# Kernel optimization log

Hardware: AMD Instinct MI355X
Metric: run time of the kernel (lower is better)

Reference implementation:

```python
import jax, jax.numpy as jnp
import numpy as np

EPS_BN = 1e-5
EPS_RENORM = 1e-9

def conv_bn_relu(x, W, g, b, m, v):
    # x: [B, Cin, N], W: [Cout, Cin] (1x1 conv, no bias). Eval-mode BN.
    y = jnp.einsum('oi,bin->bon', W, x)
    scale = (g / jnp.sqrt(v + EPS_BN))[None, :, None]
    bias = (b - m * g / jnp.sqrt(v + EPS_BN))[None, :, None]
    return jax.nn.relu(y * scale + bias)

def _make_params(key, cout, cin):
    k1, k2, k3, k4 = jax.random.split(key, 4)
    W = jax.random.normal(k1, (cout, cin), jnp.float32) * (1.0 / np.sqrt(cin))
    g = jax.random.uniform(k2, (cout,), jnp.float32, 0.5, 1.5)
    b = jax.random.normal(k3, (cout,), jnp.float32) * 0.1
    m = jax.random.normal(k4, (cout,), jnp.float32) * 0.1
    v = jax.random.uniform(jax.random.fold_in(key, 7), (cout,), jnp.float32, 0.5, 1.5)
    return W, g, b, m, v

def setup_inputs() -> dict:
    key = jax.random.key(0)
    ks = jax.random.split(key, 6)
    B, C, N = 8, 1024, 2048
    x = jax.random.normal(ks[0], (B, C, N), jnp.float32)
    inp = {'x': x}
    dims = [(1024, 1024), (1024, 1024), (128, 1024), (128, 1024), (1024, 1024)]
    for i, (co, ci) in enumerate(dims):
        W, g, b, m, v = _make_params(ks[i + 1], co, ci)
        inp[f'W{i+1}'] = W
        inp[f'g{i+1}'] = g
        inp[f'b{i+1}'] = b
        inp[f'm{i+1}'] = m
        inp[f'v{i+1}'] = v
    return inp

def reference(x,
              W1, g1, b1, m1, v1,
              W2, g2, b2, m2, v2,
              W3, g3, b3, m3, v3,
              W4, g4, b4, m4, v4,
              W5, g5, b5, m5, v5):
    x1 = conv_bn_relu(x, W1, g1, b1, m1, v1)          # [B,1024,N]
    v_ = conv_bn_relu(x1, W2, g2, b2, m2, v2)         # [B,1024,N]
    q_ = conv_bn_relu(x1, W3, g3, b3, m3, v3)         # [B,128,N]
    k_ = conv_bn_relu(x1, W4, g4, b4, m4, v4)         # [B,128,N]
    # q transposed: [B,N,128] @ [B,128,N] -> [B,N,N]
    scores = jnp.einsum('bcn,bcm->bnm', q_, k_)
    scores = jax.nn.softmax(scores, axis=-1)
    scores = scores / (EPS_RENORM + scores.sum(axis=1, keepdims=True))
    attn = jnp.einsum('bcn,bnm->bcm', v_, scores)     # [B,1024,N]
    x2 = conv_bn_relu(x1 - attn, W5, g5, b5, m5, v5)
    return x1 + x2
```

## Files before the change

kernel.cpp:

```cpp
#include <hip/hip_runtime.h>

typedef unsigned short u16;
using bf16x8 = __attribute__((ext_vector_type(8))) short;
using f32x4  = __attribute__((ext_vector_type(4))) float;

#define CH   1024
#define NP   2048
#define CQ   128

__device__ __forceinline__ float bf2f(u16 u){
  union { unsigned u; float f; } c; c.u = ((unsigned)u) << 16; return c.f;
}
__device__ __forceinline__ u16 f2bf(float f){
  unsigned x = __float_as_uint(f);
  unsigned r = (x + 0x7fffu + ((x >> 16) & 1u)) >> 16;
  return (u16)r;
}

__device__ __forceinline__ void gl2lds16(const u16* g, u16* l){
  __builtin_amdgcn_global_load_lds(
      (const __attribute__((address_space(1))) unsigned int*)(const void*)g,
      (__attribute__((address_space(3))) unsigned int*)(void*)l,
      16, 0, 0);
}

__global__ void ws_marker(float* out, float have_mb){
  out[0] = 1048576.0f + have_mb;
}

__global__ __launch_bounds__(256) void transpose_split(const float* __restrict__ x,
                                                       u16* __restrict__ xh,
                                                       u16* __restrict__ xl){
  const int bb = blockIdx.z;
  const int n0 = blockIdx.x * 64, c0 = blockIdx.y * 64;
  __shared__ float tile[64][65];
  const int t = threadIdx.x;
  const float* xb = x + ((size_t)bb*CH + c0)*NP + n0;
#pragma unroll
  for (int rr = 0; rr < 4; ++rr){
    const int c_l = (t >> 4) + rr*16;
    const int n_l = (t & 15) * 4;
    float4 v = *(const float4*)&xb[(size_t)c_l*NP + n_l];
    tile[c_l][n_l+0] = v.x; tile[c_l][n_l+1] = v.y;
    tile[c_l][n_l+2] = v.z; tile[c_l][n_l+3] = v.w;
  }
  __syncthreads();
  u16* oh = xh + ((size_t)bb*NP + n0)*CH + c0;
  u16* ol = xl + ((size_t)bb*NP + n0)*CH + c0;
#pragma unroll
  for (int rr = 0; rr < 4; ++rr){
    const int n_l = (t >> 4) + rr*16;
    const int c_l = (t & 15) * 4;
    ushort4 h, l;
    float v0 = tile[c_l+0][n_l], v1 = tile[c_l+1][n_l];
    float v2 = tile[c_l+2][n_l], v3 = tile[c_l+3][n_l];
    h.x = f2bf(v0); l.x = f2bf(v0 - bf2f(h.x));
    h.y = f2bf(v1); l.y = f2bf(v1 - bf2f(h.y));
    h.z = f2bf(v2); l.z = f2bf(v2 - bf2f(h.z));
    h.w = f2bf(v3); l.w = f2bf(v3 - bf2f(h.w));
    *(ushort4*)&oh[(size_t)n_l*CH + c_l] = h;
    *(ushort4*)&ol[(size_t)n_l*CH + c_l] = l;
  }
}

__global__ __launch_bounds__(256) void prep_all(
    const float* __restrict__ w0, const float* __restrict__ w1,
    const float* __restrict__ w2, const float* __restrict__ w3,
    const float* __restrict__ w4,
    u16* w1h, u16* w1l, u16* w2h,
    u16* w34h, u16* w34l, u16* w5h,
    const float* g3, const float* b3, const float* m3, const float* v3,
    const float* g4, const float* b4, const float* m4, const float* v4,
    float* p34, float* colsum){
  const int seg = blockIdx.y;
  if (seg == 5){
    for (int i = blockIdx.x*blockDim.x + threadIdx.x; i < 1024; i += gridDim.x*blockDim.x){
      const int grp = i >> 8, j = i & 255;
      const float* pa = (grp==0) ? g3 : (grp==1) ? b3 : (grp==2) ? m3 : v3;
      const float* pb = (grp==0) ? g4 : (grp==1) ? b4 : (grp==2) ? m4 : v4;
      p34[i] = (j < 128) ? pa[j] : pb[j-128];
    }
    return;
  }
  if (seg == 6){
    for (int i = blockIdx.x*blockDim.x + threadIdx.x; i < 8*NP; i += gridDim.x*blockDim.x)
      colsum[i] = 0.f;
    return;
  }
  const float* w; u16 *wh, *wl; int n;
  switch (seg){
    case 0:  w = w0; wh = w1h;           wl = w1l;           n = CH*CH; break;
    case 1:  w = w1; wh = w2h;           wl = nullptr;       n = CH*CH; break;
    case 2:  w = w2; wh = w34h;          wl = w34l;          n = CQ*CH; break;
    case 3:  w = w3; wh = w34h + CQ*CH;  wl = w34l + CQ*CH;  n = CQ*CH; break;
    default: w = w4; wh = w5h;           wl = nullptr;       n = CH*CH; break;
  }
  for (int i = blockIdx.x*blockDim.x + threadIdx.x; i < n; i += gridDim.x*blockDim.x){
    float v = w[i];
    u16 h = f2bf(v);
    wh[i] = h;
    if (wl) wl[i] = f2bf(v - bf2f(h));
  }
}

template<int EPI>
__global__ __launch_bounds__(512, 2) void gemm_2ph(
    const u16* __restrict__ A, const u16* __restrict__ B,
    int lda, int ldb, long astr, long bstr, int K,
    void* __restrict__ out0, long ostr, int ldo,
    const float* __restrict__ pg, const float* __restrict__ pb,
    const float* __restrict__ pm, const float* __restrict__ pv,
    const u16* __restrict__ x1h, const u16* __restrict__ x1l,
    const float* __restrict__ cinv, const u16* __restrict__ cbf)
{
  __shared__ __align__(16) u16 sA[2][16384];
  __shared__ __align__(16) u16 sB[2][16384];
  __shared__ __align__(16) u16 cl[2048];

  const int tid  = threadIdx.x;
  const int lane = tid & 63;
  const int wave = tid >> 6;
  const int wr = wave >> 1, wc = wave & 1;
  const int l15 = lane & 15, q = lane >> 4;
  const int id = blockIdx.x;
  const int bb = id & 7;
  const int rest = id >> 3;
  const int by = rest & 3;
  const int bx = rest >> 2;

  const u16* Ab = A + (size_t)bb*astr + (size_t)bx*256*lda;
  const u16* Bb = B + (size_t)bb*bstr + (size_t)by*256*ldb;

  const int sr0 = tid >> 3;
  const int sg  = (((tid & 7) ^ (sr0 & 7)) << 3);

  auto stage = [&](int kt, int bsel){
    u16* dA = sA[bsel]; u16* dB = sB[bsel];
#pragma unroll
    for (int rr = 0; rr < 4; ++rr){
      gl2lds16(Ab + (size_t)(rr*64 + sr0)*lda + kt + sg, dA + rr*4096 + tid*8);
      gl2lds16(Bb + (size_t)(rr*64 + sr0)*ldb + kt + sg, dB + rr*4096 + tid*8);
    }
  };

  int rpA[4], rpB[8];
#pragma unroll
  for (int i = 0; i < 4; ++i) rpA[i] = (wr*64 + i*16 + l15) << 6;
#pragma unroll
  for (int j = 0; j < 8; ++j) rpB[j] = (wc*128 + j*16 + l15) << 6;
  const int ckx = l15 & 7;
  const int ck0 = ((0 + q) ^ ckx) << 3;
  const int ck1 = ((4 + q) ^ ckx) << 3;

  if constexpr (EPI == 1){
    if (tid < 256)
      *(bf16x8*)&cl[tid*8] = *(const bf16x8*)&cbf[(size_t)bb*NP + tid*8];
  }

  f32x4 acc[4][8] = {};
  f32x4 accR[4] = {};

  const int NT = K >> 6;
  stage(0, 0);
  __syncthreads();

  for (int t = 0; t < NT; ++t){
    if (t + 1 < NT) stage((t + 1) << 6, (t + 1) & 1);
    const u16* cA = sA[t & 1];
    const u16* cB = sB[t & 1];
    bf16x8 af[4], bfr[8];
#pragma unroll
    for (int i = 0; i < 4; ++i) af[i]  = *(const bf16x8*)&cA[rpA[i] + ck0];
#pragma unroll
    for (int j = 0; j < 8; ++j) bfr[j] = *(const bf16x8*)&cB[rpB[j] + ck0];
    if constexpr (EPI == 1){
      const bf16x8 cbs = *(const bf16x8*)&cl[(t << 6) + q*8];
#pragma unroll
      for (int i = 0; i < 4; ++i)
        accR[i] = __builtin_amdgcn_mfma_f32_16x16x32_bf16(af[i], cbs, accR[i], 0, 0, 0);
    }
#pragma unroll
    for (int i = 0; i < 4; ++i)
#pragma unroll
      for (int j = 0; j < 8; ++j)
        acc[i][j] = __builtin_amdgcn_mfma_f32_16x16x32_bf16(af[i], bfr[j], acc[i][j], 0, 0, 0);
#pragma unroll
    for (int i = 0; i < 4; ++i) af[i]  = *(const bf16x8*)&cA[rpA[i] + ck1];
#pragma unroll
    for (int j = 0; j < 8; ++j) bfr[j] = *(const bf16x8*)&cB[rpB[j] + ck1];
    if constexpr (EPI == 1){
      const bf16x8 cbs = *(const bf16x8*)&cl[(t << 6) + 32 + q*8];
#pragma unroll
      for (int i = 0; i < 4; ++i)
        accR[i] = __builtin_amdgcn_mfma_f32_16x16x32_bf16(af[i], cbs, accR[i], 0, 0, 0);
    }
#pragma unroll
    for (int i = 0; i < 4; ++i)
#pragma unroll
      for (int j = 0; j < 8; ++j)
        acc[i][j] = __builtin_amdgcn_mfma_f32_16x16x32_bf16(af[i], bfr[j], acc[i][j], 0, 0, 0);
    __syncthreads();
  }

  const int rbase = bx*256 + wr*64;
  const int cbase = by*256 + wc*128;
#pragma unroll
  for (int j = 0; j < 8; ++j){
    const int gc = cbase + j*16 + l15;
    float scale = 0.f, bias = 0.f;
    if (EPI == 0 || EPI == 2){
      scale = pg[gc] * rsqrtf(pv[gc] + 1e-5f);
      bias  = pb[gc] - pm[gc]*scale;
    }
#pragma unroll
    for (int i = 0; i < 4; ++i){
      const int gr0 = rbase + i*16 + q*4;
      if (EPI == 0){
        const float4 cv = *(const float4*)&cinv[(size_t)bb*NP + gr0];
        ushort4 pk;
        pk.x = f2bf(fmaxf(acc[i][j][0]*scale + bias, 0.f) * cv.x);
        pk.y = f2bf(fmaxf(acc[i][j][1]*scale + bias, 0.f) * cv.y);
        pk.z = f2bf(fmaxf(acc[i][j][2]*scale + bias, 0.f) * cv.z);
        pk.w = f2bf(fmaxf(acc[i][j][3]*scale + bias, 0.f) * cv.w);
        *(ushort4*)&((u16*)out0)[(size_t)bb*ostr + (size_t)gc*ldo + gr0] = pk;
      } else if (EPI == 1){
#pragma unroll
        for (int r = 0; r < 4; ++r){
          const int gr = gr0 + r;
          const size_t idx = (size_t)bb*ostr + (size_t)gr*ldo + gc;
          const float rsv = 1.f / (1e-9f + accR[i][r]);
          const float x1v = bf2f(x1h[idx]) + bf2f(x1l[idx]);
          ((u16*)out0)[idx] = f2bf(x1v - acc[i][j][r]*rsv);
        }
      } else {
        float4 o4;
#pragma unroll
        for (int r = 0; r < 4; ++r){
          const int gr = gr0 + r;
          const size_t xidx = (size_t)bb*((size_t)NP*CH) + (size_t)gr*CH + gc;
          const float x2  = fmaxf(acc[i][j][r]*scale + bias, 0.f);
          const float x1v = bf2f(x1h[xidx]) + bf2f(x1l[xidx]);
          (&o4.x)[r] = x1v + x2;
        }
        *(float4*)&((float*)out0)[(size_t)bb*ostr + (size_t)gc*ldo + gr0] = o4;
      }
    }
  }
}

__global__ __launch_bounds__(512, 2) void gemm_split_big(
    const u16* __restrict__ Ah, const u16* __restrict__ Al,
    const u16* __restrict__ Bh, const u16* __restrict__ Bl,
    int lda, int ldb, long astr, long bstr, int K,
    u16* __restrict__ outH, u16* __restrict__ outL,
    long ostr, int ldo,
    const float* __restrict__ pg, const float* __restrict__ pb,
    const float* __restrict__ pm, const float* __restrict__ pv)
{
  __shared__ __align__(16) u16 sAh[2][8192], sAl[2][8192];
  __shared__ __align__(16) u16 sBh[2][8192], sBl[2][8192];

  const int tid  = threadIdx.x;
  const int lane = tid & 63;
  const int wave = tid >> 6;
  const int wr = wave >> 1, wc = wave & 1;
  const int l15 = lane & 15, q = lane >> 4;
  const int id = blockIdx.x;
  const int bb = id & 7;
  const int rest = id >> 3;
  const int by = rest & 3;
  const int bx = rest >> 2;

  const u16* Abh = Ah + (size_t)bb*astr + (size_t)bx*256*lda;
  const u16* Abl = Al + (size_t)bb*astr + (size_t)bx*256*lda;
  const u16* Bbh = Bh + (size_t)bb*bstr + (size_t)by*256*ldb;
  const u16* Bbl = Bl + (size_t)bb*bstr + (size_t)by*256*ldb;

  const int sr = tid >> 2;
  const int sg = (((tid & 3) ^ ((sr >> 1) & 3)) << 3);

  auto stage = [&](int kt, int bsel){
    gl2lds16(Abh + (size_t)sr*lda        + kt + sg, &sAh[bsel][tid*8]);
    gl2lds16(Abh + (size_t)(sr+128)*lda  + kt + sg, &sAh[bsel][4096 + tid*8]);
    gl2lds16(Abl + (size_t)sr*lda        + kt + sg, &sAl[bsel][tid*8]);
    gl2lds16(Abl + (size_t)(sr+128)*lda  + kt + sg, &sAl[bsel][4096 + tid*8]);
    gl2lds16(Bbh + (size_t)sr*ldb        + kt + sg, &sBh[bsel][tid*8]);
    gl2lds16(Bbh + (size_t)(sr+128)*ldb  + kt + sg, &sBh[bsel][4096 + tid*8]);
    gl2lds16(Bbl + (size_t)sr*ldb        + kt + sg, &sBl[bsel][tid*8]);
    gl2lds16(Bbl + (size_t)(sr+128)*ldb  + kt + sg, &sBl[bsel][4096 + tid*8]);
  };

  int offA[4], offB[8];
#pragma unroll
  for (int i = 0; i < 4; ++i){
    const int ra = wr*64 + i*16 + l15;
    offA[i] = ra*32 + ((q ^ ((ra >> 1) & 3)) << 3);
  }
#pragma unroll
  for (int j = 0; j < 8; ++j){
    const int rb = wc*128 + j*16 + l15;
    offB[j] = rb*32 + ((q ^ ((rb >> 1) & 3)) << 3);
  }

  f32x4 acc[4][8] = {};

  const int NT = K >> 5;
  stage(0, 0);
  __syncthreads();

  for (int t = 0; t < NT; ++t){
    if (t + 1 < NT) stage((t + 1) << 5, (t + 1) & 1);
    const int cur = t & 1;
    bf16x8 ah[4], al2[4];
#pragma unroll
    for (int i = 0; i < 4; ++i){
      ah[i]  = *(const bf16x8*)&sAh[cur][offA[i]];
      al2[i] = *(const bf16x8*)&sAl[cur][offA[i]];
    }
#pragma unroll
    for (int jh = 0; jh < 2; ++jh){
      bf16x8 bh[4], bl[4];
#pragma unroll
      for (int j = 0; j < 4; ++j){
        bh[j] = *(const bf16x8*)&sBh[cur][offB[jh*4 + j]];
        bl[j] = *(const bf16x8*)&sBl[cur][offB[jh*4 + j]];
      }
#pragma unroll
      for (int i = 0; i < 4; ++i)
#pragma unroll
        for (int j = 0; j < 4; ++j){
          acc[i][jh*4+j] = __builtin_amdgcn_mfma_f32_16x16x32_bf16(ah[i],  bh[j], acc[i][jh*4+j], 0, 0, 0);
          acc[i][jh*4+j] = __builtin_amdgcn_mfma_f32_16x16x32_bf16(ah[i],  bl[j], acc[i][jh*4+j], 0, 0, 0);
          acc[i][jh*4+j] = __builtin_amdgcn_mfma_f32_16x16x32_bf16(al2[i], bh[j], acc[i][jh*4+j], 0, 0, 0);
        }
    }
    __syncthreads();
  }

  const int rbase = bx*256 + wr*64;
  const int cbase = by*256 + wc*128;
#pragma unroll
  for (int j = 0; j < 8; ++j){
    const int gc = cbase + j*16 + l15;
    const float scale = pg[gc] * rsqrtf(pv[gc] + 1e-5f);
    const float bias  = pb[gc] - pm[gc]*scale;
#pragma unroll
    for (int i = 0; i < 4; ++i){
      const int gr0 = rbase + i*16 + q*4;
#pragma unroll
      for (int r = 0; r < 4; ++r){
        const size_t idx = (size_t)bb*ostr + (size_t)(gr0 + r)*ldo + gc;
        const float y = fmaxf(acc[i][j][r]*scale + bias, 0.f);
        const u16 h = f2bf(y);
        outH[idx] = h;
        outL[idx] = f2bf(y - bf2f(h));
      }
    }
  }
}

template<int EPI>
__global__ __launch_bounds__(256, 4) void gemm_split3(
    const u16* __restrict__ Ah, const u16* __restrict__ Al,
    const u16* __restrict__ Bh, const u16* __restrict__ Bl,
    int lda, int ldb, long astr, long bstr, int K,
    u16* __restrict__ outH, u16* __restrict__ outL,
    long ostr, int ldo,
    const float* __restrict__ pg, const float* __restrict__ pb,
    const float* __restrict__ pm, const float* __restrict__ pv,
    float* __restrict__ colsum, int gymask, int gyshift)
{
  __shared__ __align__(16) u16 sAh[4096], sAl[4096], sBh[4096], sBl[4096];
  const int tid  = threadIdx.x;
  const int lane = tid & 63, wave = tid >> 6;
  const int wr = wave & 1, wc = wave >> 1;
  const int l15 = lane & 15, q = lane >> 4;
  const int id = blockIdx.x;
  const int bb = id & 7;
  const int rest = id >> 3;
  const int by = rest & gymask;
  const int bx = rest >> gyshift;
  const u16* Abh = Ah + (size_t)bb*astr + (size_t)bx*128*lda;
  const u16* Abl = Al + (size_t)bb*astr + (size_t)bx*128*lda;
  const u16* Bbh = Bh + (size_t)bb*bstr + (size_t)by*128*ldb;
  const u16* Bbl = Bl + (size_t)bb*bstr + (size_t)by*128*ldb;

  f32x4 acc[4][4] = {};

  const int r0 = tid >> 2, r1 = r0 + 64;
  const int cs = (((tid & 3) ^ ((r0 >> 1) & 3)) << 3);

  int offA[4], offB[4];
#pragma unroll
  for (int i = 0; i < 4; ++i){
    const int ra = wr*64 + i*16 + l15;
    offA[i] = ra*32 + ((q ^ ((ra >> 1) & 3)) << 3);
    const int rb = wc*64 + i*16 + l15;
    offB[i] = rb*32 + ((q ^ ((rb >> 1) & 3)) << 3);
  }

  for (int kt = 0; kt < K; kt += 32){
    gl2lds16(Abh + (size_t)r0*lda + kt + cs, &sAh[tid*8]);
    gl2lds16(Abh + (size_t)r1*lda + kt + cs, &sAh[2048 + tid*8]);
    gl2lds16(Abl + (size_t)r0*lda + kt + cs, &sAl[tid*8]);
    gl2lds16(Abl + (size_t)r1*lda + kt + cs, &sAl[2048 + tid*8]);
    gl2lds16(Bbh + (size_t)r0*ldb + kt + cs, &sBh[tid*8]);
    gl2lds16(Bbh + (size_t)r1*ldb + kt + cs, &sBh[2048 + tid*8]);
    gl2lds16(Bbl + (size_t)r0*ldb + kt + cs, &sBl[tid*8]);
    gl2lds16(Bbl + (size_t)r1*ldb + kt + cs, &sBl[2048 + tid*8]);
    __syncthreads();
    bf16x8 ah[4], al[4], bh2[4], bl2[4];
#pragma unroll
    for (int i = 0; i < 4; ++i){
      ah[i] = *(const bf16x8*)&sAh[offA[i]];
      al[i] = *(const bf16x8*)&sAl[offA[i]];
    }
#pragma unroll
    for (int j = 0; j < 4; ++j){
      bh2[j] = *(const bf16x8*)&sBh[offB[j]];
      bl2[j] = *(const bf16x8*)&sBl[offB[j]];
    }
#pragma unroll
    for (int i = 0; i < 4; ++i)
#pragma unroll
      for (int j = 0; j < 4; ++j){
        acc[i][j] = __builtin_amdgcn_mfma_f32_16x16x32_bf16(ah[i], bh2[j], acc[i][j], 0, 0, 0);
        acc[i][j] = __builtin_amdgcn_mfma_f32_16x16x32_bf16(ah[i], bl2[j], acc[i][j], 0, 0, 0);
        acc[i][j] = __builtin_amdgcn_mfma_f32_16x16x32_bf16(al[i], bh2[j], acc[i][j], 0, 0, 0);
      }
    __syncthreads();
  }

  const int rbase = bx*128 + wr*64;
  const int cbase = by*128 + wc*64;

  if constexpr (EPI == 1){
    __shared__ float colpart[128];
    if (tid < 128) colpart[tid] = 0.f;
    __syncthreads();
#pragma unroll
    for (int j = 0; j < 4; ++j){
      const int gc = cbase + j*16 + l15;
      float lsum = 0.f;
#pragma unroll
      for (int i = 0; i < 4; ++i){
        const int gr0 = rbase + i*16 + q*4;
#pragma unroll
        for (int r = 0; r < 4; ++r){
          const float e = __expf(fminf(acc[i][j][r], 85.f));
          outH[(size_t)bb*ostr + (size_t)(gr0 + r)*ldo + gc] = f2bf(e);
          lsum += e;
        }
      }
      atomicAdd(&colpart[wc*64 + j*16 + l15], lsum);
    }
    __syncthreads();
    if (tid < 128) atomicAdd(&colsum[(size_t)bb*NP + (size_t)by*128 + tid], colpart[tid]);
  } else {
#pragma unroll
    for (int j = 0; j < 4; ++j){
      const int gc = cbase + j*16 + l15;
      const float scale = pg[gc] * rsqrtf(pv[gc] + 1e-5f);
      const float bias  = pb[gc] - pm[gc]*scale;
#pragma unroll
      for (int i = 0; i < 4; ++i){
        const int gr0 = rbase + i*16 + q*4;
#pragma unroll
        for (int r = 0; r < 4; ++r){
          const size_t idx = (size_t)bb*ostr + (size_t)(gr0 + r)*ldo + gc;
          const float y = fmaxf(acc[i][j][r]*scale + bias, 0.f);
          const u16 h = f2bf(y);
          outH[idx] = h;
          outL[idx] = f2bf(y - bf2f(h));
        }
      }
    }
  }
}

__global__ __launch_bounds__(256) void colinv_k(const float* __restrict__ cs,
                                                float* __restrict__ ci,
                                                u16* __restrict__ cib, int n){
  const int i = blockIdx.x*blockDim.x + threadIdx.x;
  if (i < n){
    const float v = 1.0f / cs[i];
    ci[i]  = v;
    cib[i] = f2bf(v);
  }
}

extern "C" void kernel_launch(void* const* d_in, const int* in_sizes, int n_in,
                              void* d_out, int out_size, void* d_ws, size_t ws_size,
                              hipStream_t stream){
  const float* x = (const float*)d_in[0];
  const float *W[5], *g[5], *bt[5], *mu[5], *vr[5];
  for (int i = 0; i < 5; ++i){
    W[i]  = (const float*)d_in[1 + 5*i + 0];
    g[i]  = (const float*)d_in[1 + 5*i + 1];
    bt[i] = (const float*)d_in[1 + 5*i + 2];
    mu[i] = (const float*)d_in[1 + 5*i + 3];
    vr[i] = (const float*)d_in[1 + 5*i + 4];
  }

  char* wp = (char*)d_ws;
  size_t off = 0;
  auto take = [&](size_t bytes) -> void* {
    void* p = wp + off;
    off = (off + bytes + 255) & ~(size_t)255;
    return p;
  };
  u16*   xh   = (u16*)take(33554432);
  u16*   xl   = (u16*)take(33554432);
  u16*   x1h  = (u16*)take(33554432);
  u16*   x1l  = (u16*)take(33554432);
  u16*   qkh  = (u16*)take(8388608);
  u16*   qkl  = (u16*)take(8388608);
  float* csum = (float*)take(65536);
  float* cinv = (float*)take(65536);
  u16*   cibf = (u16*)take(32768);
  u16*   w1h  = (u16*)take(2097152);
  u16*   w1l  = (u16*)take(2097152);
  u16*   w2h  = (u16*)take(2097152);
  u16*   w34h = (u16*)take(524288);
  u16*   w34l = (u16*)take(524288);
  u16*   w5h  = (u16*)take(2097152);
  float* p34  = (float*)take(4096);

  if (ws_size < off){
    ws_marker<<<1, 1, 0, stream>>>((float*)d_out, (float)(ws_size >> 20));
    return;
  }

  u16* vh   = xh;
  u16* tt   = xl;
  u16* expS = (u16*)d_out;

  prep_all<<<dim3(256, 7), 256, 0, stream>>>(
      W[0], W[1], W[2], W[3], W[4],
      w1h, w1l, w2h, w34h, w34l, w5h,
      g[2], bt[2], mu[2], vr[2], g[3], bt[3], mu[3], vr[3],
      p34, csum);

  transpose_split<<<dim3(32,16,8), 256, 0, stream>>>(x, xh, xl);

  gemm_split_big<<<dim3(256), 512, 0, stream>>>(
      xh, xl, w1h, w1l, CH, CH, (long)NP*CH, 0, CH,
      x1h, x1l, (long)NP*CH, CH, g[0], bt[0], mu[0], vr[0]);

  gemm_split3<0><<<dim3(256), 256, 0, stream>>>(
      x1h, x1l, w34h, w34l, CH, CH, (long)NP*CH, 0, CH,
      qkh, qkl, (long)NP*256, 256, p34, p34+256, p34+512, p34+768, nullptr, 1, 1);

  gemm_split3<1><<<dim3(2048), 256, 0, stream>>>(
      qkh + 128, qkl + 128, qkh, qkl, 256, 256, (long)NP*256, (long)NP*256, CQ,
      expS, nullptr, (long)NP*NP, NP,
      nullptr, nullptr, nullptr, nullptr, csum, 15, 4);

  colinv_k<<<dim3(64), 256, 0, stream>>>(csum, cinv, cibf, 8*NP);

  gemm_2ph<0><<<dim3(256), 512, 0, stream>>>(
      x1h, w2h, CH, CH, (long)NP*CH, 0, CH,
      vh, (long)CH*NP, NP, g[1], bt[1], mu[1], vr[1],
      nullptr, nullptr, cinv, nullptr);

  gemm_2ph<1><<<dim3(256), 512, 0, stream>>>(
      expS, vh, NP, NP, (long)NP*NP, (long)CH*NP, NP,
      tt, (long)NP*CH, CH, nullptr, nullptr, nullptr, nullptr,
      x1h, x1l, nullptr, cibf);

  gemm_2ph<2><<<dim3(256), 512, 0, stream>>>(
      tt, w5h, CH, CH, (long)NP*CH, 0, CH,
      d_out, (long)CH*NP, NP, g[4], bt[4], mu[4], vr[4],
      x1h, x1l, nullptr, nullptr);
}
```

Measured before the change: 599.1 us.

## Restructure bf16 GEMM into 8-wave ping-pong schedule with half-tile staged loads

```diff
diff --git a/kernel.cpp b/kernel.cpp
--- a/kernel.cpp
+++ b/kernel.cpp
@@ -104,7 +104,7 @@
 }
 
 template<int EPI>
-__global__ __launch_bounds__(512, 2) void gemm_2ph(
+__global__ __launch_bounds__(512, 2) void gemm_8b(
     const u16* __restrict__ A, const u16* __restrict__ B,
     int lda, int ldb, long astr, long bstr, int K,
     void* __restrict__ out0, long ostr, int ldo,
@@ -113,14 +113,14 @@
     const u16* __restrict__ x1h, const u16* __restrict__ x1l,
     const float* __restrict__ cinv, const u16* __restrict__ cbf)
 {
-  __shared__ __align__(16) u16 sA[2][16384];
-  __shared__ __align__(16) u16 sB[2][16384];
+  __shared__ __align__(16) u16 sA[2][2][8192];
+  __shared__ __align__(16) u16 sB[2][2][8192];
   __shared__ __align__(16) u16 cl[2048];
 
   const int tid  = threadIdx.x;
   const int lane = tid & 63;
   const int wave = tid >> 6;
-  const int wr = wave >> 1, wc = wave & 1;
+  const int wr = wave >> 2, wc = wave & 3;
   const int l15 = lane & 15, q = lane >> 4;
   const int id = blockIdx.x;
   const int bb = id & 7;
@@ -131,81 +131,172 @@
   const u16* Ab = A + (size_t)bb*astr + (size_t)bx*256*lda;
   const u16* Bb = B + (size_t)bb*bstr + (size_t)by*256*ldb;
 
-  const int sr0 = tid >> 3;
-  const int sg  = (((tid & 7) ^ (sr0 & 7)) << 3);
-
-  auto stage = [&](int kt, int bsel){
-    u16* dA = sA[bsel]; u16* dB = sB[bsel];
-#pragma unroll
-    for (int rr = 0; rr < 4; ++rr){
-      gl2lds16(Ab + (size_t)(rr*64 + sr0)*lda + kt + sg, dA + rr*4096 + tid*8);
-      gl2lds16(Bb + (size_t)(rr*64 + sr0)*ldb + kt + sg, dB + rr*4096 + tid*8);
-    }
+  const int sr = tid >> 3;
+  const int sg = (((tid & 7) ^ (sr & 7)) << 3);
+
+  auto stA = [&](int half, int T){
+    u16* d = &sA[T & 1][half][0];
+    const u16* s = Ab + (size_t)(half*128 + sr)*lda + T*64 + sg;
+    gl2lds16(s, d + tid*8);
+    gl2lds16(s + (size_t)64*lda, d + 4096 + tid*8);
   };
-
-  int rpA[4], rpB[8];
-#pragma unroll
-  for (int i = 0; i < 4; ++i) rpA[i] = (wr*64 + i*16 + l15) << 6;
-#pragma unroll
-  for (int j = 0; j < 8; ++j) rpB[j] = (wc*128 + j*16 + l15) << 6;
-  const int ckx = l15 & 7;
-  const int ck0 = ((0 + q) ^ ckx) << 3;
-  const int ck1 = ((4 + q) ^ ckx) << 3;
+  auto stB = [&](int half, int T){
+    u16* d = &sB[T & 1][half][0];
+    const u16* s = Bb + (size_t)(half*128 + sr)*ldb + T*64 + sg;
+    gl2lds16(s, d + tid*8);
+    gl2lds16(s + (size_t)64*ldb, d + 4096 + tid*8);
+  };
+
+  int rA[8], rB[4];
+#pragma unroll
+  for (int f = 0; f < 8; ++f) rA[f] = (f*16 + l15) << 6;
+#pragma unroll
+  for (int n = 0; n < 4; ++n) rB[n] = (((wc & 1) << 6) + n*16 + l15) << 6;
+  const int ckk0 = ((q)     ^ (l15 & 7)) << 3;
+  const int ckk1 = ((4 + q) ^ (l15 & 7)) << 3;
 
   if constexpr (EPI == 1){
     if (tid < 256)
       *(bf16x8*)&cl[tid*8] = *(const bf16x8*)&cbf[(size_t)bb*NP + tid*8];
-  }
-
-  f32x4 acc[4][8] = {};
-  f32x4 accR[4] = {};
+    __syncthreads();
+  }
+
+  f32x4 acc[8][4] = {};
+  f32x4 accR[8] = {};
 
   const int NT = K >> 6;
-  stage(0, 0);
-  __syncthreads();
-
-  for (int t = 0; t < NT; ++t){
-    if (t + 1 < NT) stage((t + 1) << 6, (t + 1) & 1);
-    const u16* cA = sA[t & 1];
-    const u16* cB = sB[t & 1];
-    bf16x8 af[4], bfr[8];
-#pragma unroll
-    for (int i = 0; i < 4; ++i) af[i]  = *(const bf16x8*)&cA[rpA[i] + ck0];
-#pragma unroll
-    for (int j = 0; j < 8; ++j) bfr[j] = *(const bf16x8*)&cB[rpB[j] + ck0];
+  stA(0, 0); stA(1, 0); stB(0, 0); stB(1, 0);
+  if (NT > 1){
+    stA(0, 1);
+    asm volatile("s_waitcnt vmcnt(2)" ::: "memory");
+  } else {
+    asm volatile("s_waitcnt vmcnt(0)" ::: "memory");
+  }
+  __builtin_amdgcn_s_barrier();
+
+  for (int U = 0; U < NT; ++U){
+    const int p = U & 1;
+    const u16* a0 = &sA[p][wr][0];
+    const u16* b0 = &sB[p][wc >> 1][0];
+    bf16x8 af[2][4], bfr[2][2], cbs0, cbs1;
+
+#pragma unroll
+    for (int f = 0; f < 4; ++f){
+      af[0][f] = *(const bf16x8*)&a0[rA[f] + ckk0];
+      af[1][f] = *(const bf16x8*)&a0[rA[f] + ckk1];
+    }
+#pragma unroll
+    for (int n = 0; n < 2; ++n){
+      bfr[0][n] = *(const bf16x8*)&b0[rB[n] + ckk0];
+      bfr[1][n] = *(const bf16x8*)&b0[rB[n] + ckk1];
+    }
     if constexpr (EPI == 1){
-      const bf16x8 cbs = *(const bf16x8*)&cl[(t << 6) + q*8];
-#pragma unroll
-      for (int i = 0; i < 4; ++i)
-        accR[i] = __builtin_amdgcn_mfma_f32_16x16x32_bf16(af[i], cbs, accR[i], 0, 0, 0);
-    }
-#pragma unroll
-    for (int i = 0; i < 4; ++i)
-#pragma unroll
-      for (int j = 0; j < 8; ++j)
-        acc[i][j] = __builtin_amdgcn_mfma_f32_16x16x32_bf16(af[i], bfr[j], acc[i][j], 0, 0, 0);
-#pragma unroll
-    for (int i = 0; i < 4; ++i) af[i]  = *(const bf16x8*)&cA[rpA[i] + ck1];
-#pragma unroll
-    for (int j = 0; j < 8; ++j) bfr[j] = *(const bf16x8*)&cB[rpB[j] + ck1];
+      cbs0 = *(const bf16x8*)&cl[(U << 6) + q*8];
+      cbs1 = *(const bf16x8*)&cl[(U << 6) + 32 + q*8];
+    }
+    if (U + 1 < NT) stA(1, U + 1);
+    __builtin_amdgcn_sched_barrier(0);
+    __builtin_amdgcn_s_barrier();
+    asm volatile("s_waitcnt lgkmcnt(0)" ::: "memory");
+    __builtin_amdgcn_sched_barrier(0);
+    __builtin_amdgcn_s_setprio(1);
     if constexpr (EPI == 1){
-      const bf16x8 cbs = *(const bf16x8*)&cl[(t << 6) + 32 + q*8];
-#pragma unroll
-      for (int i = 0; i < 4; ++i)
-        accR[i] = __builtin_amdgcn_mfma_f32_16x16x32_bf16(af[i], cbs, accR[i], 0, 0, 0);
-    }
-#pragma unroll
-    for (int i = 0; i < 4; ++i)
-#pragma unroll
-      for (int j = 0; j < 8; ++j)
-        acc[i][j] = __builtin_amdgcn_mfma_f32_16x16x32_bf16(af[i], bfr[j], acc[i][j], 0, 0, 0);
-    __syncthreads();
-  }
-
-  const int rbase = bx*256 + wr*64;
-  const int cbase = by*256 + wc*128;
-#pragma unroll
-  for (int j = 0; j < 8; ++j){
+#pragma unroll
+      for (int f = 0; f < 4; ++f){
+        accR[f] = __builtin_amdgcn_mfma_f32_16x16x32_bf16(af[0][f], cbs0, accR[f], 0, 0, 0);
+        accR[f] = __builtin_amdgcn_mfma_f32_16x16x32_bf16(af[1][f], cbs1, accR[f], 0, 0, 0);
+      }
+    }
+#pragma unroll
+    for (int kk = 0; kk < 2; ++kk)
+#pragma unroll
+      for (int f = 0; f < 4; ++f)
+#pragma unroll
+        for (int n = 0; n < 2; ++n)
+          acc[f][n] = __builtin_amdgcn_mfma_f32_16x16x32_bf16(af[kk][f], bfr[kk][n], acc[f][n], 0, 0, 0);
+    __builtin_amdgcn_s_setprio(0);
+    __builtin_amdgcn_s_barrier();
+
+#pragma unroll
+    for (int n = 0; n < 2; ++n){
+      bfr[0][n] = *(const bf16x8*)&b0[rB[2 + n] + ckk0];
+      bfr[1][n] = *(const bf16x8*)&b0[rB[2 + n] + ckk1];
+    }
+    if (U + 1 < NT) stB(0, U + 1);
+    __builtin_amdgcn_sched_barrier(0);
+    __builtin_amdgcn_s_barrier();
+    asm volatile("s_waitcnt lgkmcnt(0)" ::: "memory");
+    __builtin_amdgcn_sched_barrier(0);
+    __builtin_amdgcn_s_setprio(1);
+#pragma unroll
+    for (int kk = 0; kk < 2; ++kk)
+#pragma unroll
+      for (int f = 0; f < 4; ++f)
+#pragma unroll
+        for (int n = 0; n < 2; ++n)
+          acc[f][2+n] = __builtin_amdgcn_mfma_f32_16x16x32_bf16(af[kk][f], bfr[kk][n], acc[f][2+n], 0, 0, 0);
+    __builtin_amdgcn_s_setprio(0);
+    __builtin_amdgcn_s_barrier();
+
+#pragma unroll
+    for (int f = 0; f < 4; ++f){
+      af[0][f] = *(const bf16x8*)&a0[rA[4 + f] + ckk0];
+      af[1][f] = *(const bf16x8*)&a0[rA[4 + f] + ckk1];
+    }
+    if (U + 1 < NT) stB(1, U + 1);
+    __builtin_amdgcn_sched_barrier(0);
+    __builtin_amdgcn_s_barrier();
+    asm volatile("s_waitcnt lgkmcnt(0)" ::: "memory");
+    __builtin_amdgcn_sched_barrier(0);
+    __builtin_amdgcn_s_setprio(1);
+    if constexpr (EPI == 1){
+#pragma unroll
+      for (int f = 0; f < 4; ++f){
+        accR[4+f] = __builtin_amdgcn_mfma_f32_16x16x32_bf16(af[0][f], cbs0, accR[4+f], 0, 0, 0);
+        accR[4+f] = __builtin_amdgcn_mfma_f32_16x16x32_bf16(af[1][f], cbs1, accR[4+f], 0, 0, 0);
+      }
+    }
+#pragma unroll
+    for (int kk = 0; kk < 2; ++kk)
+#pragma unroll
+      for (int f = 0; f < 4; ++f)
+#pragma unroll
+        for (int n = 0; n < 2; ++n)
+          acc[4+f][2+n] = __builtin_amdgcn_mfma_f32_16x16x32_bf16(af[kk][f], bfr[kk][n], acc[4+f][2+n], 0, 0, 0);
+    __builtin_amdgcn_s_setprio(0);
+    __builtin_amdgcn_s_barrier();
+
+#pragma unroll
+    for (int n = 0; n < 2; ++n){
+      bfr[0][n] = *(const bf16x8*)&b0[rB[n] + ckk0];
+      bfr[1][n] = *(const bf16x8*)&b0[rB[n] + ckk1];
+    }
+    if (U + 2 < NT){
+      stA(0, U + 2);
+      asm volatile("s_waitcnt vmcnt(2)" ::: "memory");
+    } else {
+      asm volatile("s_waitcnt vmcnt(0)" ::: "memory");
+    }
+    __builtin_amdgcn_sched_barrier(0);
+    __builtin_amdgcn_s_barrier();
+    asm volatile("s_waitcnt lgkmcnt(0)" ::: "memory");
+    __builtin_amdgcn_sched_barrier(0);
+    __builtin_amdgcn_s_setprio(1);
+#pragma unroll
+    for (int kk = 0; kk < 2; ++kk)
+#pragma unroll
+      for (int f = 0; f < 4; ++f)
+#pragma unroll
+        for (int n = 0; n < 2; ++n)
+          acc[4+f][n] = __builtin_amdgcn_mfma_f32_16x16x32_bf16(af[kk][f], bfr[kk][n], acc[4+f][n], 0, 0, 0);
+    __builtin_amdgcn_s_setprio(0);
+    __builtin_amdgcn_s_barrier();
+  }
+
+  const int rbase = bx*256 + wr*128;
+  const int cbase = by*256 + wc*64;
+#pragma unroll
+  for (int j = 0; j < 4; ++j){
     const int gc = cbase + j*16 + l15;
     float scale = 0.f, bias = 0.f;
     if (EPI == 0 || EPI == 2){
@@ -213,7 +304,7 @@
       bias  = pb[gc] - pm[gc]*scale;
     }
 #pragma unroll
-    for (int i = 0; i < 4; ++i){
+    for (int i = 0; i < 8; ++i){
       const int gr0 = rbase + i*16 + q*4;
       if (EPI == 0){
         const float4 cv = *(const float4*)&cinv[(size_t)bb*NP + gr0];
@@ -558,17 +649,17 @@
 
   colinv_k<<<dim3(64), 256, 0, stream>>>(csum, cinv, cibf, 8*NP);
 
-  gemm_2ph<0><<<dim3(256), 512, 0, stream>>>(
+  gemm_8b<0><<<dim3(256), 512, 0, stream>>>(
       x1h, w2h, CH, CH, (long)NP*CH, 0, CH,
       vh, (long)CH*NP, NP, g[1], bt[1], mu[1], vr[1],
       nullptr, nullptr, cinv, nullptr);
 
-  gemm_2ph<1><<<dim3(256), 512, 0, stream>>>(
+  gemm_8b<1><<<dim3(256), 512, 0, stream>>>(
       expS, vh, NP, NP, (long)NP*NP, (long)CH*NP, NP,
       tt, (long)NP*CH, CH, nullptr, nullptr, nullptr, nullptr,
       x1h, x1l, nullptr, cibf);
 
-  gemm_2ph<2><<<dim3(256), 512, 0, stream>>>(
+  gemm_8b<2><<<dim3(256), 512, 0, stream>>>(
       tt, w5h, CH, CH, (long)NP*CH, 0, CH,
       d_out, (long)CH*NP, NP, g[4], bt[4], mu[4], vr[4],
       x1h, x1l, nullptr, nullptr);
```

Result: slower. 678.5 us (+13.3%).

## Add 256x128-tile single-precision GEMM kernel for conv2 and conv5 launches

Applied to the files above, without the earlier changes.

```diff
diff --git a/kernel.cpp b/kernel.cpp
--- a/kernel.cpp
+++ b/kernel.cpp
@@ -232,6 +232,107 @@
           const float x1v = bf2f(x1h[idx]) + bf2f(x1l[idx]);
           ((u16*)out0)[idx] = f2bf(x1v - acc[i][j][r]*rsv);
         }
+      } else {
+        float4 o4;
+#pragma unroll
+        for (int r = 0; r < 4; ++r){
+          const int gr = gr0 + r;
+          const size_t xidx = (size_t)bb*((size_t)NP*CH) + (size_t)gr*CH + gc;
+          const float x2  = fmaxf(acc[i][j][r]*scale + bias, 0.f);
+          const float x1v = bf2f(x1h[xidx]) + bf2f(x1l[xidx]);
+          (&o4.x)[r] = x1v + x2;
+        }
+        *(float4*)&((float*)out0)[(size_t)bb*ostr + (size_t)gc*ldo + gr0] = o4;
+      }
+    }
+  }
+}
+
+template<int EPI>
+__global__ __launch_bounds__(512, 4) void gemm_n128(
+    const u16* __restrict__ A, const u16* __restrict__ B,
+    int lda, int ldb, long astr, long bstr, int K,
+    void* __restrict__ out0, long ostr, int ldo,
+    const float* __restrict__ pg, const float* __restrict__ pb,
+    const float* __restrict__ pm, const float* __restrict__ pv,
+    const u16* __restrict__ x1h, const u16* __restrict__ x1l,
+    const float* __restrict__ cinv)
+{
+  __shared__ __align__(16) u16 sA[2][8192];
+  __shared__ __align__(16) u16 sB[2][4096];
+
+  const int tid  = threadIdx.x;
+  const int lane = tid & 63;
+  const int wave = tid >> 6;
+  const int wr = wave >> 1, wc = wave & 1;
+  const int l15 = lane & 15, q = lane >> 4;
+  const int id = blockIdx.x;
+  const int bb = id & 7;
+  const int rest = id >> 3;
+  const int by = rest & 7;
+  const int bx = rest >> 3;
+
+  const u16* Ab = A + (size_t)bb*astr + (size_t)bx*256*lda;
+  const u16* Bb = B + (size_t)bb*bstr + (size_t)by*128*ldb;
+
+  const int sr = tid >> 2;
+  const int sg = (((tid & 3) ^ ((sr >> 1) & 3)) << 3);
+
+  auto stage = [&](int kt, int bsel){
+    gl2lds16(Ab + (size_t)sr*lda        + kt + sg, &sA[bsel][tid*8]);
+    gl2lds16(Ab + (size_t)(sr+128)*lda  + kt + sg, &sA[bsel][4096 + tid*8]);
+    gl2lds16(Bb + (size_t)sr*ldb        + kt + sg, &sB[bsel][tid*8]);
+  };
+
+  int offA[4], offB[4];
+#pragma unroll
+  for (int i = 0; i < 4; ++i){
+    const int ra = wr*64 + i*16 + l15;
+    offA[i] = ra*32 + ((q ^ ((ra >> 1) & 3)) << 3);
+    const int rb = wc*64 + i*16 + l15;
+    offB[i] = rb*32 + ((q ^ ((rb >> 1) & 3)) << 3);
+  }
+
+  f32x4 acc[4][4] = {};
+
+  const int NT = K >> 5;
+  stage(0, 0);
+  __syncthreads();
+
+  for (int t = 0; t < NT; ++t){
+    if (t + 1 < NT) stage((t + 1) << 5, (t + 1) & 1);
+    const int cur = t & 1;
+    bf16x8 ah[4], bh[4];
+#pragma unroll
+    for (int i = 0; i < 4; ++i) ah[i] = *(const bf16x8*)&sA[cur][offA[i]];
+#pragma unroll
+    for (int j = 0; j < 4; ++j) bh[j] = *(const bf16x8*)&sB[cur][offB[j]];
+#pragma unroll
+    for (int i = 0; i < 4; ++i)
+#pragma unroll
+      for (int j = 0; j < 4; ++j)
+        acc[i][j] = __builtin_amdgcn_mfma_f32_16x16x32_bf16(ah[i], bh[j], acc[i][j], 0, 0, 0);
+    __syncthreads();
+  }
+
+  const int rbase = bx*256 + wr*64;
+  const int cbase = by*128 + wc*64;
+#pragma unroll
+  for (int j = 0; j < 4; ++j){
+    const int gc = cbase + j*16 + l15;
+    const float scale = pg[gc] * rsqrtf(pv[gc] + 1e-5f);
+    const float bias  = pb[gc] - pm[gc]*scale;
+#pragma unroll
+    for (int i = 0; i < 4; ++i){
+      const int gr0 = rbase + i*16 + q*4;
+      if (EPI == 0){
+        const float4 cv = *(const float4*)&cinv[(size_t)bb*NP + gr0];
+        ushort4 pk;
+        pk.x = f2bf(fmaxf(acc[i][j][0]*scale + bias, 0.f) * cv.x);
+        pk.y = f2bf(fmaxf(acc[i][j][1]*scale + bias, 0.f) * cv.y);
+        pk.z = f2bf(fmaxf(acc[i][j][2]*scale + bias, 0.f) * cv.z);
+        pk.w = f2bf(fmaxf(acc[i][j][3]*scale + bias, 0.f) * cv.w);
+        *(ushort4*)&((u16*)out0)[(size_t)bb*ostr + (size_t)gc*ldo + gr0] = pk;
       } else {
         float4 o4;
 #pragma unroll
@@ -558,18 +659,18 @@
 
   colinv_k<<<dim3(64), 256, 0, stream>>>(csum, cinv, cibf, 8*NP);
 
-  gemm_2ph<0><<<dim3(256), 512, 0, stream>>>(
+  gemm_n128<0><<<dim3(512), 512, 0, stream>>>(
       x1h, w2h, CH, CH, (long)NP*CH, 0, CH,
       vh, (long)CH*NP, NP, g[1], bt[1], mu[1], vr[1],
-      nullptr, nullptr, cinv, nullptr);
+      nullptr, nullptr, cinv);
 
   gemm_2ph<1><<<dim3(256), 512, 0, stream>>>(
       expS, vh, NP, NP, (long)NP*NP, (long)CH*NP, NP,
       tt, (long)NP*CH, CH, nullptr, nullptr, nullptr, nullptr,
       x1h, x1l, nullptr, cibf);
 
-  gemm_2ph<2><<<dim3(256), 512, 0, stream>>>(
+  gemm_n128<2><<<dim3(512), 512, 0, stream>>>(
       tt, w5h, CH, CH, (long)NP*CH, 0, CH,
       d_out, (long)CH*NP, NP, g[4], bt[4], mu[4], vr[4],
-      x1h, x1l, nullptr, nullptr);
-}
+      x1h, x1l, nullptr);
+}
```

Result: slower. 626.5 us (+4.6%).

## Split-K the Q/K projection GEMM with atomic accumulation and finalize pass

Applied to the files above, without the earlier changes.

```diff
diff --git a/kernel.cpp b/kernel.cpp
--- a/kernel.cpp
+++ b/kernel.cpp
@@ -103,6 +103,11 @@
   }
 }
 
+__global__ __launch_bounds__(256) void zero_f4(float4* __restrict__ p, int n4){
+  const int i = blockIdx.x*blockDim.x + threadIdx.x;
+  if (i < n4) p[i] = make_float4(0.f, 0.f, 0.f, 0.f);
+}
+
 template<int EPI>
 __global__ __launch_bounds__(512, 2) void gemm_2ph(
     const u16* __restrict__ A, const u16* __restrict__ B,
@@ -357,6 +362,115 @@
       }
     }
   }
+}
+
+__global__ __launch_bounds__(256, 4) void gemm_split_ksum(
+    const u16* __restrict__ Ah, const u16* __restrict__ Al,
+    const u16* __restrict__ Bh, const u16* __restrict__ Bl,
+    float* __restrict__ out)
+{
+  __shared__ __align__(16) u16 sAh[4096], sAl[4096], sBh[4096], sBl[4096];
+  const int tid  = threadIdx.x;
+  const int lane = tid & 63, wave = tid >> 6;
+  const int wr = wave & 1, wc = wave >> 1;
+  const int l15 = lane & 15, q = lane >> 4;
+  const int id = blockIdx.x;
+  const int bb = id & 7;
+  const int rest = id >> 3;
+  const int kc = rest & 3;
+  const int r2 = rest >> 2;
+  const int by = r2 & 1;
+  const int bx = r2 >> 1;
+  const int koff = kc << 8;
+
+  const u16* Abh = Ah + (size_t)bb*((size_t)NP*CH) + (size_t)bx*128*CH;
+  const u16* Abl = Al + (size_t)bb*((size_t)NP*CH) + (size_t)bx*128*CH;
+  const u16* Bbh = Bh + (size_t)by*128*CH;
+  const u16* Bbl = Bl + (size_t)by*128*CH;
+
+  f32x4 acc[4][4] = {};
+
+  const int r0 = tid >> 2, r1 = r0 + 64;
+  const int cs = (((tid & 3) ^ ((r0 >> 1) & 3)) << 3);
+
+  int offA[4], offB[4];
+#pragma unroll
+  for (int i = 0; i < 4; ++i){
+    const int ra = wr*64 + i*16 + l15;
+    offA[i] = ra*32 + ((q ^ ((ra >> 1) & 3)) << 3);
+    const int rb = wc*64 + i*16 + l15;
+    offB[i] = rb*32 + ((q ^ ((rb >> 1) & 3)) << 3);
+  }
+
+  for (int kt = 0; kt < 256; kt += 32){
+    const int kk = koff + kt;
+    gl2lds16(Abh + (size_t)r0*CH + kk + cs, &sAh[tid*8]);
+    gl2lds16(Abh + (size_t)r1*CH + kk + cs, &sAh[2048 + tid*8]);
+    gl2lds16(Abl + (size_t)r0*CH + kk + cs, &sAl[tid*8]);
+    gl2lds16(Abl + (size_t)r1*CH + kk + cs, &sAl[2048 + tid*8]);
+    gl2lds16(Bbh + (size_t)r0*CH + kk + cs, &sBh[tid*8]);
+    gl2lds16(Bbh + (size_t)r1*CH + kk + cs, &sBh[2048 + tid*8]);
+    gl2lds16(Bbl + (size_t)r0*CH + kk + cs, &sBl[tid*8]);
+    gl2lds16(Bbl + (size_t)r1*CH + kk + cs, &sBl[2048 + tid*8]);
+    __syncthreads();
+    bf16x8 ah[4], al[4], bh2[4], bl2[4];
+#pragma unroll
+    for (int i = 0; i < 4; ++i){
+      ah[i] = *(const bf16x8*)&sAh[offA[i]];
+      al[i] = *(const bf16x8*)&sAl[offA[i]];
+    }
+#pragma unroll
+    for (int j = 0; j < 4; ++j){
+      bh2[j] = *(const bf16x8*)&sBh[offB[j]];
+      bl2[j] = *(const bf16x8*)&sBl[offB[j]];
+    }
+#pragma unroll
+    for (int i = 0; i < 4; ++i)
+#pragma unroll
+      for (int j = 0; j < 4; ++j){
+        acc[i][j] = __builtin_amdgcn_mfma_f32_16x16x32_bf16(ah[i], bh2[j], acc[i][j], 0, 0, 0);
+        acc[i][j] = __builtin_amdgcn_mfma_f32_16x16x32_bf16(ah[i], bl2[j], acc[i][j], 0, 0, 0);
+        acc[i][j] = __builtin_amdgcn_mfma_f32_16x16x32_bf16(al[i], bh2[j], acc[i][j], 0, 0, 0);
+      }
+    __syncthreads();
+  }
+
+  const int rbase = bx*128 + wr*64;
+  const int cbase = by*128 + wc*64;
+#pragma unroll
+  for (int j = 0; j < 4; ++j){
+    const int gc = cbase + j*16 + l15;
+#pragma unroll
+    for (int i = 0; i < 4; ++i){
+      const int gr0 = rbase + i*16 + q*4;
+#pragma unroll
+      for (int r = 0; r < 4; ++r)
+        atomicAdd(&out[(size_t)bb*((size_t)NP*256) + (size_t)(gr0 + r)*256 + gc],
+                  acc[i][j][r]);
+    }
+  }
+}
+
+__global__ __launch_bounds__(256) void qk_fin(const float* __restrict__ acc,
+                                              const float* __restrict__ p34,
+                                              u16* __restrict__ qh,
+                                              u16* __restrict__ ql){
+  const int idx = blockIdx.x*256 + threadIdx.x;
+  const int j0 = (idx*4) & 255;
+  const float4 a = ((const float4*)acc)[idx];
+  ushort4 h, l;
+#pragma unroll
+  for (int r = 0; r < 4; ++r){
+    const int j = j0 + r;
+    const float scale = p34[j] * rsqrtf(p34[768 + j] + 1e-5f);
+    const float bias  = p34[256 + j] - p34[512 + j]*scale;
+    const float y = fmaxf((&a.x)[r]*scale + bias, 0.f);
+    const u16 hh = f2bf(y);
+    (&h.x)[r] = hh;
+    (&l.x)[r] = f2bf(y - bf2f(hh));
+  }
+  ((ushort4*)qh)[idx] = h;
+  ((ushort4*)ql)[idx] = l;
 }
 
 template<int EPI>
@@ -531,9 +645,10 @@
     return;
   }
 
-  u16* vh   = xh;
-  u16* tt   = xl;
-  u16* expS = (u16*)d_out;
+  u16*   vh     = xh;
+  u16*   tt     = xl;
+  float* qk_acc = (float*)xh;
+  u16*   expS   = (u16*)d_out;
 
   prep_all<<<dim3(256, 7), 256, 0, stream>>>(
       W[0], W[1], W[2], W[3], W[4],
@@ -547,9 +662,10 @@
       xh, xl, w1h, w1l, CH, CH, (long)NP*CH, 0, CH,
       x1h, x1l, (long)NP*CH, CH, g[0], bt[0], mu[0], vr[0]);
 
-  gemm_split3<0><<<dim3(256), 256, 0, stream>>>(
-      x1h, x1l, w34h, w34l, CH, CH, (long)NP*CH, 0, CH,
-      qkh, qkl, (long)NP*256, 256, p34, p34+256, p34+512, p34+768, nullptr, 1, 1);
+  zero_f4<<<dim3(4096), 256, 0, stream>>>((float4*)qk_acc, 8*NP*256/4);
+  gemm_split_ksum<<<dim3(1024), 256, 0, stream>>>(
+      x1h, x1l, w34h, w34l, qk_acc);
+  qk_fin<<<dim3(4096), 256, 0, stream>>>(qk_acc, p34, qkh, qkl);
 
   gemm_split3<1><<<dim3(2048), 256, 0, stream>>>(
       qkh + 128, qkl + 128, qkh, qkl, 256, 256, (long)NP*256, (long)NP*256, CQ,
```

Result: slower. 644.3 us (+7.6%).
